# Kernel optimization log

Hardware: AMD Instinct MI355X
Metric: run time of the kernel (lower is better)

Reference implementation:

```python
import jax, jax.numpy as jnp
import numpy as np

B, S, HID = 4, 2048, 2048
H, HKV, D = 16, 4, 128
RANK = 512
SCALE = D ** -0.5


def setup_inputs() -> dict:
    key = jax.random.key(0)
    ks = jax.random.split(key, 5)
    scale_w = 0.02
    return {
        "hidden_states": jax.random.normal(ks[0], (B, S, HID), dtype=jnp.float32),
        "Wq": jax.random.normal(ks[1], (HID, H * D), dtype=jnp.float32) * scale_w,
        "Wc": jax.random.normal(ks[2], (HID, RANK), dtype=jnp.float32) * scale_w,
        "Wup": jax.random.normal(ks[3], (RANK, HKV * D), dtype=jnp.float32) * scale_w,
        "Wo": jax.random.normal(ks[4], (H * D, HID), dtype=jnp.float32) * scale_w,
    }


def reference(hidden_states, Wq, Wc, Wup, Wo):
    b, s, _ = hidden_states.shape
    n_rep = H // HKV
    # Q projection -> (b, H, s, D)
    q = (hidden_states @ Wq).reshape(b, s, H, D).transpose(0, 2, 1, 3)
    # low-rank KV compression -> (b, s, RANK)
    kv_c = hidden_states @ Wc
    # gate in source is ones -> sigmoid(1) constant scalar multiply
    kv_c = kv_c * jax.nn.sigmoid(jnp.float32(1.0))
    # decompress: single kv_up_proj produces shared K/V content
    kv = (kv_c @ Wup).reshape(b, s, HKV, D).transpose(0, 2, 1, 3)  # (b, HKV, s, D)
    k = jnp.repeat(kv, n_rep, axis=1)  # (b, H, s, D), repeat_interleave over heads
    v = k
    scores = jnp.einsum("bhqd,bhkd->bhqk", q, k) * SCALE
    attn = jax.nn.softmax(scores.astype(jnp.float32), axis=-1).astype(q.dtype)
    out = jnp.einsum("bhqk,bhkd->bhqd", attn, v)
    out = out.transpose(0, 2, 1, 3).reshape(b, s, H * D)
    return out @ Wo
```

## Files before the change

### kernel.cpp

```cpp
#include <hip/hip_runtime.h>
#include <hip/hip_bf16.h>
#include <stdint.h>

#define DEV __device__ __forceinline__

typedef __bf16 bf16x8 __attribute__((ext_vector_type(8)));
typedef float f32x4 __attribute__((ext_vector_type(4)));
typedef float f32x16 __attribute__((ext_vector_type(16)));
typedef int i32x4 __attribute__((ext_vector_type(4)));


DEV void gload_lds16(const void* g, void* l) {
  __builtin_amdgcn_global_load_lds((const __attribute__((address_space(1))) void*)g,
                                   (__attribute__((address_space(3))) void*)l, 16, 0, 0);
}

__global__ __launch_bounds__(256) void k_cast(const float* __restrict__ in,
                                              __hip_bfloat16* __restrict__ out, int n) {
  int i = (blockIdx.x * 256 + threadIdx.x) * 8;
  if (i >= n) return;
  const float4* p = (const float4*)(in + i);
  float4 a = p[0], c = p[1];
  bf16x8 v;
  v[0] = (__bf16)a.x; v[1] = (__bf16)a.y; v[2] = (__bf16)a.z; v[3] = (__bf16)a.w;
  v[4] = (__bf16)c.x; v[5] = (__bf16)c.y; v[6] = (__bf16)c.z; v[7] = (__bf16)c.w;
  *(bf16x8*)(out + i) = v;
}

__global__ __launch_bounds__(256) void k_tcast(const float* __restrict__ in,
                                               __hip_bfloat16* __restrict__ out, int R, int C) {
  __shared__ float t[32][33];
  int c0 = blockIdx.x * 32, r0 = blockIdx.y * 32;
  int x = threadIdx.x, y0 = threadIdx.y;
  for (int j = y0; j < 32; j += 8) t[j][x] = in[(size_t)(r0 + j) * C + c0 + x];
  __syncthreads();
  for (int j = y0; j < 32; j += 8)
    out[(size_t)(c0 + j) * R + r0 + x] = __float2bfloat16(t[x][j]);
}

__global__ __launch_bounds__(256) void k_tbf16(const __hip_bfloat16* __restrict__ in,
                                               __hip_bfloat16* __restrict__ out) {
  __shared__ unsigned short t[32][33];
  int z = blockIdx.z;
  const unsigned short* ip = (const unsigned short*)in + (size_t)z * 2048 * 128;
  unsigned short* op = (unsigned short*)out + (size_t)z * 2048 * 128;
  int d0 = blockIdx.x * 32, s0 = blockIdx.y * 32;
  int x = threadIdx.x, y0 = threadIdx.y;
  for (int j = y0; j < 32; j += 8) t[j][x] = ip[(size_t)(s0 + j) * 128 + d0 + x];
  __syncthreads();
  for (int j = y0; j < 32; j += 8) op[(size_t)(d0 + j) * 2048 + s0 + x] = t[x][j];
}

template <int MODE>
__global__ __launch_bounds__(256, 2) void k_gemm(const __hip_bfloat16* __restrict__ A,
                                                 const __hip_bfloat16* __restrict__ BT,
                                                 void* __restrict__ Cout,
                                                 int M, int N, int K, float scale) {
  __shared__ __align__(16) __hip_bfloat16 As[128 * 64];
  __shared__ __align__(16) __hip_bfloat16 Bs[128 * 64];
  const int tid = threadIdx.x;
  const int lane = tid & 63, wid = tid >> 6;
  const int g = lane >> 4, lr = lane & 15;
  const int m0 = blockIdx.x * 128, n0 = blockIdx.y * 128;
  const int wr = wid >> 1, wc = wid & 1;
  const f32x4 vzero = {0.f, 0.f, 0.f, 0.f};

  f32x4 acc[4][4];
#pragma unroll
  for (int i = 0; i < 4; ++i)
#pragma unroll
    for (int j = 0; j < 4; ++j) acc[i][j] = vzero;

  const char* aSrc[4];
  const char* bSrc[4];
  char* aDst[4];
  char* bDst[4];
#pragma unroll
  for (int i = 0; i < 4; ++i) {
    int p = i * 4096 + tid * 16;
    int row = p >> 7, colb = p & 127;
    int scol = colb ^ ((row & 7) << 4);
    aSrc[i] = (const char*)A + ((size_t)(m0 + row) * K) * 2 + scol;
    bSrc[i] = (const char*)BT + ((size_t)(n0 + row) * K) * 2 + scol;
    aDst[i] = (char*)As + i * 4096 + wid * 1024;
    bDst[i] = (char*)Bs + i * 4096 + wid * 1024;
  }

  const int nk = K >> 6;
  for (int kt = 0; kt < nk; ++kt) {
    const size_t ko = (size_t)kt * 128;
#pragma unroll
    for (int i = 0; i < 4; ++i) gload_lds16(aSrc[i] + ko, aDst[i]);
#pragma unroll
    for (int i = 0; i < 4; ++i) gload_lds16(bSrc[i] + ko, bDst[i]);
    __syncthreads();
#pragma unroll
    for (int kc = 0; kc < 2; ++kc) {
      bf16x8 af[4], bfr[4];
#pragma unroll
      for (int fm = 0; fm < 4; ++fm) {
        int row = wr * 64 + fm * 16 + lr;
        int cb = (kc * 64 + g * 16) ^ ((row & 7) << 4);
        af[fm] = *(const bf16x8*)((const char*)As + row * 128 + cb);
      }
#pragma unroll
      for (int fn = 0; fn < 4; ++fn) {
        int row = wc * 64 + fn * 16 + lr;
        int cb = (kc * 64 + g * 16) ^ ((row & 7) << 4);
        bfr[fn] = *(const bf16x8*)((const char*)Bs + row * 128 + cb);
      }
#pragma unroll
      for (int fm = 0; fm < 4; ++fm)
#pragma unroll
        for (int fn = 0; fn < 4; ++fn)
          acc[fm][fn] =
              __builtin_amdgcn_mfma_f32_16x16x32_bf16(af[fm], bfr[fn], acc[fm][fn], 0, 0, 0);
    }
    __syncthreads();
  }

#pragma unroll
  for (int fm = 0; fm < 4; ++fm) {
#pragma unroll
    for (int fn = 0; fn < 4; ++fn) {
      const int mb = m0 + wr * 64 + fm * 16 + g * 4;
      const int n = n0 + wc * 64 + fn * 16 + lr;
#pragma unroll
      for (int r = 0; r < 4; ++r) {
        float v = acc[fm][fn][r] * scale;
        int m = mb + r;
        if constexpr (MODE == 2) {
          int b = m >> 11, s = m & 2047, hk = n >> 7, d = n & 127;
          ((__hip_bfloat16*)Cout)[(((size_t)(b * 4 + hk) * 2048) + s) * 128 + d] =
              __float2bfloat16(v);
        } else {
          ((__hip_bfloat16*)Cout)[(size_t)n * M + m] = __float2bfloat16(v);
        }
      }
    }
  }
}

template <int MODE>
__global__ __launch_bounds__(512, 2) void k_gemm256(const __hip_bfloat16* __restrict__ A,
                                                    const __hip_bfloat16* __restrict__ BT,
                                                    void* __restrict__ Cout,
                                                    int M, int N, int K, float scale) {
  __shared__ __align__(16) char smem[131072];
  const int tid = threadIdx.x;
  const int lane = tid & 63, wid = tid >> 6;
  const int lr = lane & 15, g = lane >> 4;
  const int m0 = blockIdx.x * 256, n0 = blockIdx.y * 256;
  const int wr = wid >> 2, wc = wid & 3;
  const size_t K2 = (size_t)K * 2;
  const f32x4 vzero = {0.f, 0.f, 0.f, 0.f};

  const char *sA0, *sA1, *sB0, *sB1;
  {
    int p = tid * 16;
    int row = p >> 6;
    int slot = (p >> 4) & 3;
    int sw = (slot ^ ((row >> 1) & 3)) << 4;
    sA0 = (const char*)A + (size_t)(m0 + row) * K2 + sw;
    sA1 = (const char*)A + (size_t)(m0 + row + 128) * K2 + sw;
    sB0 = (const char*)BT + (size_t)(n0 + row) * K2 + sw;
    sB1 = (const char*)BT + (size_t)(n0 + row + 128) * K2 + sw;
  }
  char* const ldsW = smem + wid * 1024;

  auto stA = [&](int buf, int kc, size_t koT) {
    char* hb = ldsW + buf * 65536 + kc * 16384;
    gload_lds16(sA0 + koT + (kc << 6), hb);
    gload_lds16(sA1 + koT + (kc << 6), hb + 8192);
  };
  auto stB = [&](int buf, int kc, size_t koT) {
    char* hb = ldsW + buf * 65536 + 32768 + kc * 16384;
    gload_lds16(sB0 + koT + (kc << 6), hb);
    gload_lds16(sB1 + koT + (kc << 6), hb + 8192);
  };

  const int swr = ((g ^ ((lr >> 1) & 3)) << 4);
  const char* rdA = smem + wr * 8192 + lr * 64 + swr;
  const char* rdB = smem + 32768 + wc * 4096 + lr * 64 + swr;

  f32x4 acc[8][4];
#pragma unroll
  for (int i = 0; i < 8; ++i)
#pragma unroll
    for (int j = 0; j < 4; ++j) acc[i][j] = vzero;

  stA(0, 0, 0); stB(0, 0, 0); stA(0, 1, 0); stB(0, 1, 0);

  auto mfma16 = [&](bf16x8* af, bf16x8* bfv, int mh) {
    __builtin_amdgcn_s_setprio(1);
#pragma unroll
    for (int f = 0; f < 4; ++f)
#pragma unroll
      for (int n = 0; n < 4; ++n)
        acc[mh * 4 + f][n] =
            __builtin_amdgcn_mfma_f32_16x16x32_bf16(af[f], bfv[n], acc[mh * 4 + f][n], 0, 0, 0);
    __builtin_amdgcn_s_setprio(0);
  };

  auto tileK = [&](int buf, size_t koNext, bool doStage, bool last) {
    asm volatile("s_waitcnt vmcnt(4)" ::: "memory");
    __builtin_amdgcn_s_barrier();
    bf16x8 a[4], b[4];
    if (doStage) stA(buf ^ 1, 0, koNext);
#pragma unroll
    for (int n = 0; n < 4; ++n) b[n] = *(const bf16x8*)(rdB + buf * 65536 + n * 1024);
#pragma unroll
    for (int f = 0; f < 4; ++f) a[f] = *(const bf16x8*)(rdA + buf * 65536 + f * 1024);
    asm volatile("s_waitcnt lgkmcnt(0)" ::: "memory");
    __builtin_amdgcn_sched_barrier(0);
    mfma16(a, b, 0);
    if (doStage) stB(buf ^ 1, 0, koNext);
#pragma unroll
    for (int f = 0; f < 4; ++f) a[f] = *(const bf16x8*)(rdA + buf * 65536 + 4096 + f * 1024);
    asm volatile("s_waitcnt lgkmcnt(0)" ::: "memory");
    __builtin_amdgcn_sched_barrier(0);
    mfma16(a, b, 1);
    if (last) {
      asm volatile("s_waitcnt vmcnt(0)" ::: "memory");
    } else {
      asm volatile("s_waitcnt vmcnt(4)" ::: "memory");
    }
    __builtin_amdgcn_s_barrier();
    if (doStage) stA(buf ^ 1, 1, koNext);
#pragma unroll
    for (int n = 0; n < 4; ++n) b[n] = *(const bf16x8*)(rdB + buf * 65536 + 16384 + n * 1024);
#pragma unroll
    for (int f = 0; f < 4; ++f) a[f] = *(const bf16x8*)(rdA + buf * 65536 + 16384 + f * 1024);
    asm volatile("s_waitcnt lgkmcnt(0)" ::: "memory");
    __builtin_amdgcn_sched_barrier(0);
    mfma16(a, b, 0);
    if (doStage) stB(buf ^ 1, 1, koNext);
#pragma unroll
    for (int f = 0; f < 4; ++f)
      a[f] = *(const bf16x8*)(rdA + buf * 65536 + 16384 + 4096 + f * 1024);
    asm volatile("s_waitcnt lgkmcnt(0)" ::: "memory");
    __builtin_amdgcn_sched_barrier(0);
    mfma16(a, b, 1);
  };

  const int nk = K >> 6;
  size_t ko = 128;
#pragma unroll 1
  for (int it = 0; it < (nk - 2) / 2; ++it) {
    tileK(0, ko, true, false); ko += 128;
    tileK(1, ko, true, false); ko += 128;
  }
  tileK(0, ko, true, false);
  tileK(1, 0, false, true);

#pragma unroll
  for (int fm = 0; fm < 8; ++fm) {
#pragma unroll
    for (int fn = 0; fn < 4; ++fn) {
      const int mb = m0 + wr * 128 + fm * 16 + g * 4;
      const int n = n0 + wc * 64 + fn * 16 + lr;
#pragma unroll
      for (int r = 0; r < 4; ++r) {
        float v = acc[fm][fn][r] * scale;
        int m = mb + r;
        if constexpr (MODE == 0) {
          ((float*)Cout)[(size_t)m * N + n] = v;
        } else {
          int b = m >> 11, s = m & 2047, h = n >> 7, d = n & 127;
          ((__hip_bfloat16*)Cout)[(((size_t)(b * 16 + h) * 2048) + s) * 128 + d] =
              __float2bfloat16(v);
        }
      }
    }
  }
}

__global__ __launch_bounds__(512, 2) void k_attn2(const __hip_bfloat16* __restrict__ q,
                                                  const __hip_bfloat16* __restrict__ kv,
                                                  const __hip_bfloat16* __restrict__ kvT,
                                                  __hip_bfloat16* __restrict__ out) {
  __shared__ __align__(16) char smem[65536];
  const int tid = threadIdx.x, lane = tid & 63, wid = tid >> 6;
  const int hi = lane >> 5, lq = lane & 31;
  const int qt = blockIdx.x;
  const int pair = blockIdx.y;
  const int b = pair >> 2, hkv = pair & 3;
  const int h = hkv * 4 + (wid & 3);
  const int q0w = qt * 64 + (wid >> 2) * 32;

  const char* qrow =
      (const char*)q + (((size_t)(b * 16 + h) * 2048 + q0w + lq) * 128 + hi * 8) * 2;
  bf16x8 qfr[8];
#pragma unroll
  for (int kt = 0; kt < 8; ++kt) qfr[kt] = *(const bf16x8*)(qrow + kt * 32);

  const char* kbase = (const char*)kv + ((size_t)pair * 2048 * 128) * 2;
  const char* tbase = (const char*)kvT + ((size_t)pair * 2048 * 128) * 2;
  const char* pK;
  const char* pV;
  {
    int p0 = tid * 16;
    int krow = p0 >> 8, kcol = p0 & 255;
    pK = kbase + (size_t)krow * 256 + (kcol ^ ((krow & 15) << 4));
    int vrow = p0 >> 7, vcol = p0 & 127;
    pV = tbase + (size_t)vrow * 4096 + (vcol ^ ((vrow & 7) << 4));
  }

  f32x16 accO[4];
#pragma unroll
  for (int dt = 0; dt < 4; ++dt)
#pragma unroll
    for (int i = 0; i < 16; ++i) accO[dt][i] = 0.f;
  float m_run = -1e30f, l_run = 0.f;

  const int hsK = (hi * 16) ^ ((lq & 15) << 4);
  const int hsV = (hi * 16) ^ ((lq & 7) << 4);

  auto stage = [&](int kb, int vb) {
    gload_lds16(pK, smem + kb + wid * 1024);
    gload_lds16(pK + 8192, smem + kb + 8192 + wid * 1024);
    gload_lds16(pV, smem + vb + wid * 1024);
    gload_lds16(pV + 262144, smem + vb + 8192 + wid * 1024);
    pK += 16384;
    pV += 128;
  };

  auto compute = [&](int kb, int vb) {
    f32x16 st[2];
#pragma unroll
    for (int i = 0; i < 16; ++i) { st[0][i] = 0.f; st[1][i] = 0.f; }
    const char* Kb = smem + kb;
#pragma unroll
    for (int tau = 0; tau < 2; ++tau) {
      const char* Kr = Kb + (tau * 32 + lq) * 256;
#pragma unroll
      for (int kt = 0; kt < 8; ++kt) {
        bf16x8 kf = *(const bf16x8*)(Kr + ((kt * 32) ^ hsK));
        st[tau] = __builtin_amdgcn_mfma_f32_32x32x16_bf16(kf, qfr[kt], st[tau], 0, 0, 0);
      }
    }
    float mloc[8];
#pragma unroll
    for (int i = 0; i < 8; ++i)
      mloc[i] = fmaxf(fmaxf(st[0][i], st[0][i + 8]), fmaxf(st[1][i], st[1][i + 8]));
#pragma unroll
    for (int i = 0; i < 4; ++i) mloc[i] = fmaxf(mloc[i], mloc[i + 4]);
    float pm = fmaxf(fmaxf(mloc[0], mloc[1]), fmaxf(mloc[2], mloc[3]));
    pm = fmaxf(pm, __shfl_xor(pm, 32));
    if (__any(pm > m_run + 8.f)) {
      float mnew = fmaxf(m_run, pm);
      float alpha = __builtin_amdgcn_exp2f(m_run - mnew);
      m_run = mnew;
      l_run *= alpha;
#pragma unroll
      for (int dt = 0; dt < 4; ++dt)
#pragma unroll
        for (int i = 0; i < 16; ++i) accO[dt][i] *= alpha;
    }
    float p0[16], p1[16];
#pragma unroll
    for (int i = 0; i < 16; ++i) p0[i] = __builtin_amdgcn_exp2f(st[0][i] - m_run);
#pragma unroll
    for (int i = 0; i < 16; ++i) p1[i] = __builtin_amdgcn_exp2f(st[1][i] - m_run);
    float s0 = 0.f, s1 = 0.f, s2 = 0.f, s3 = 0.f;
#pragma unroll
    for (int i = 0; i < 8; ++i) {
      s0 += p0[i]; s1 += p0[i + 8]; s2 += p1[i]; s3 += p1[i + 8];
    }
    l_run += (s0 + s1) + (s2 + s3);
    bf16x8 pfr[4];
#pragma unroll
    for (int ks = 0; ks < 4; ++ks) {
      const int base = (ks & 1) * 8;
      int A0, A1, B0, B1;
      if (ks < 2) {
        asm("v_cvt_pk_bf16_f32 %0, %1, %2" : "=v"(A0) : "v"(p0[base + 0]), "v"(p0[base + 1]));
        asm("v_cvt_pk_bf16_f32 %0, %1, %2" : "=v"(A1) : "v"(p0[base + 2]), "v"(p0[base + 3]));
        asm("v_cvt_pk_bf16_f32 %0, %1, %2" : "=v"(B0) : "v"(p0[base + 4]), "v"(p0[base + 5]));
        asm("v_cvt_pk_bf16_f32 %0, %1, %2" : "=v"(B1) : "v"(p0[base + 6]), "v"(p0[base + 7]));
      } else {
        asm("v_cvt_pk_bf16_f32 %0, %1, %2" : "=v"(A0) : "v"(p1[base + 0]), "v"(p1[base + 1]));
        asm("v_cvt_pk_bf16_f32 %0, %1, %2" : "=v"(A1) : "v"(p1[base + 2]), "v"(p1[base + 3]));
        asm("v_cvt_pk_bf16_f32 %0, %1, %2" : "=v"(B0) : "v"(p1[base + 4]), "v"(p1[base + 5]));
        asm("v_cvt_pk_bf16_f32 %0, %1, %2" : "=v"(B1) : "v"(p1[base + 6]), "v"(p1[base + 7]));
      }
      asm("v_permlane32_swap_b32 %0, %1" : "+v"(A0), "+v"(B0));
      asm("v_permlane32_swap_b32 %0, %1" : "+v"(A1), "+v"(B1));
      union { int w[4]; bf16x8 v; } u;
      u.w[0] = A0; u.w[1] = A1; u.w[2] = B0; u.w[3] = B1;
      pfr[ks] = u.v;
    }
    const char* Vb = smem + vb;
#pragma unroll
    for (int dt = 0; dt < 4; ++dt) {
      const char* Vr = Vb + (dt * 32 + lq) * 128;
#pragma unroll
      for (int ks = 0; ks < 4; ++ks) {
        bf16x8 vf = *(const bf16x8*)(Vr + ((ks * 32) ^ hsV));
        accO[dt] = __builtin_amdgcn_mfma_f32_32x32x16_bf16(vf, pfr[ks], accO[dt], 0, 0, 0);
      }
    }
  };

  stage(0, 32768);
  __syncthreads();
#pragma unroll 1
  for (int it = 0; it < 16; ++it) {
    stage(16384, 49152);
    compute(0, 32768);
    __syncthreads();
    if (it < 15) stage(0, 32768);
    compute(16384, 49152);
    __syncthreads();
  }

  float lt = l_run + __shfl_xor(l_run, 32);
  float inv = 1.f / lt;
#pragma unroll
  for (int dt = 0; dt < 4; ++dt)
#pragma unroll
    for (int i = 0; i < 16; ++i) accO[dt][i] *= inv;

  __syncthreads();
  char* scr = smem + wid * 8192;
  const int swq = (lq & 15) << 4;
#pragma unroll
  for (int dt = 0; dt < 4; ++dt) {
#pragma unroll
    for (int rp = 0; rp < 8; ++rp) {
      int w;
      asm("v_cvt_pk_bf16_f32 %0, %1, %2"
          : "=v"(w)
          : "v"(accO[dt][2 * rp]), "v"(accO[dt][2 * rp + 1]));
      int dloc = ((2 * rp) & 3) + 8 * (rp >> 1) + 4 * hi;
      int bytec = (dt * 64 + dloc * 2) ^ swq;
      *(int*)(scr + lq * 256 + bytec) = w;
    }
  }
  __syncthreads();
  const int l16 = lane & 15, lh = lane >> 4;
#pragma unroll
  for (int ps = 0; ps < 8; ++ps) {
    int qr = ps * 4 + lh;
    i32x4 v = *(const i32x4*)(scr + qr * 256 + ((l16 * 16) ^ ((qr & 15) << 4)));
    char* dst = (char*)out + (((size_t)(b * 2048 + q0w + qr) * 2048) + h * 128 + l16 * 8) * 2;
    *(i32x4*)dst = v;
  }
}

extern "C" void kernel_launch(void* const* d_in, const int* in_sizes, int n_in,
                              void* d_out, int out_size, void* d_ws, size_t ws_size,
                              hipStream_t stream) {
  const float* hs = (const float*)d_in[0];
  const float* Wq = (const float*)d_in[1];
  const float* Wc = (const float*)d_in[2];
  const float* Wup = (const float*)d_in[3];
  const float* Wo = (const float*)d_in[4];

  if (ws_size < 105381888u) return;
  char* ws = (char*)d_ws;
  __hip_bfloat16* hs_bf = (__hip_bfloat16*)(ws + 0);
  __hip_bfloat16* q_attn = (__hip_bfloat16*)(ws + 33554432);
  __hip_bfloat16* kvb = (__hip_bfloat16*)(ws + 67108864);
  __hip_bfloat16* kvT = (__hip_bfloat16*)(ws + 75497472);
  __hip_bfloat16* WqT = (__hip_bfloat16*)(ws + 83886080);
  __hip_bfloat16* WoT = (__hip_bfloat16*)(ws + 92274688);
  __hip_bfloat16* WupT = (__hip_bfloat16*)(ws + 100663296);
  __hip_bfloat16* Wc_bf = (__hip_bfloat16*)(ws + 101187584);
  __hip_bfloat16* WckvT = (__hip_bfloat16*)(ws + 103284736);
  __hip_bfloat16* attnout = hs_bf;

  const float qscale = (float)(0.08838834764831845 * 1.4426950408889634);

  k_cast<<<8192, 256, 0, stream>>>(hs, hs_bf, 16777216);
  k_cast<<<512, 256, 0, stream>>>(Wc, Wc_bf, 1048576);
  k_tcast<<<dim3(64, 64), dim3(32, 8), 0, stream>>>(Wq, WqT, 2048, 2048);
  k_tcast<<<dim3(64, 64), dim3(32, 8), 0, stream>>>(Wo, WoT, 2048, 2048);
  k_tcast<<<dim3(16, 16), dim3(32, 8), 0, stream>>>(Wup, WupT, 512, 512);
  k_gemm<3><<<dim3(16, 4), 256, 0, stream>>>(Wc_bf, WupT, WckvT, 2048, 512, 512,
                                             0.7310585786300049f);
  k_gemm256<1><<<dim3(32, 8), 512, 0, stream>>>(hs_bf, WqT, q_attn, 8192, 2048, 2048, qscale);
  k_gemm<2><<<dim3(64, 4), 256, 0, stream>>>(hs_bf, WckvT, kvb, 8192, 512, 2048, 1.0f);
  k_tbf16<<<dim3(4, 64, 16), dim3(32, 8), 0, stream>>>(kvb, kvT);
  k_attn2<<<dim3(32, 16), 512, 0, stream>>>(q_attn, kvb, kvT, attnout);
  k_gemm256<0><<<dim3(32, 8), 512, 0, stream>>>(attnout, WoT, d_out, 8192, 2048, 2048, 1.0f);
}
```

Baseline: 350.8 us.

## Restructure 256x256 GEMM LDS layout, pipeline quadrants, and swizzle block order

New measurement: 353.5 us. Within noise of the previous version (+0.8%).

```diff
diff --git a/kernel.cpp b/kernel.cpp
--- a/kernel.cpp
+++ b/kernel.cpp
@@ -150,38 +150,32 @@
   const int tid = threadIdx.x;
   const int lane = tid & 63, wid = tid >> 6;
   const int lr = lane & 15, g = lane >> 4;
-  const int m0 = blockIdx.x * 256, n0 = blockIdx.y * 256;
+  const int bid = blockIdx.x;
+  const int swz = (bid & 7) * 32 + (bid >> 3);
+  const int m0 = (swz & 31) * 256, n0 = (swz >> 5) * 256;
   const int wr = wid >> 2, wc = wid & 3;
   const size_t K2 = (size_t)K * 2;
   const f32x4 vzero = {0.f, 0.f, 0.f, 0.f};
 
-  const char *sA0, *sA1, *sB0, *sB1;
-  {
-    int p = tid * 16;
-    int row = p >> 6;
-    int slot = (p >> 4) & 3;
-    int sw = (slot ^ ((row >> 1) & 3)) << 4;
-    sA0 = (const char*)A + (size_t)(m0 + row) * K2 + sw;
-    sA1 = (const char*)A + (size_t)(m0 + row + 128) * K2 + sw;
-    sB0 = (const char*)BT + (size_t)(n0 + row) * K2 + sw;
-    sB1 = (const char*)BT + (size_t)(n0 + row + 128) * K2 + sw;
-  }
+  const int srow = tid >> 3, sslot = tid & 7;
+  const int sw = (sslot ^ (srow & 7)) << 4;
+  const char* gA = (const char*)A + (size_t)(m0 + srow) * K2 + sw;
+  const char* gB = (const char*)BT + (size_t)(n0 + srow) * K2 + sw;
+  const size_t hG = (size_t)128 * K2;
+  const size_t r2 = (size_t)64 * K2;
   char* const ldsW = smem + wid * 1024;
 
-  auto stA = [&](int buf, int kc, size_t koT) {
-    char* hb = ldsW + buf * 65536 + kc * 16384;
-    gload_lds16(sA0 + koT + (kc << 6), hb);
-    gload_lds16(sA1 + koT + (kc << 6), hb + 8192);
-  };
-  auto stB = [&](int buf, int kc, size_t koT) {
-    char* hb = ldsW + buf * 65536 + 32768 + kc * 16384;
-    gload_lds16(sB0 + koT + (kc << 6), hb);
-    gload_lds16(sB1 + koT + (kc << 6), hb + 8192);
-  };
-
-  const int swr = ((g ^ ((lr >> 1) & 3)) << 4);
-  const char* rdA = smem + wr * 8192 + lr * 64 + swr;
-  const char* rdB = smem + 32768 + wc * 4096 + lr * 64 + swr;
+  auto stage = [&](int buf, int half, int isB, size_t koB) {
+    const char* src = (isB ? gB : gA) + (half ? hG : 0) + koB;
+    char* dst = ldsW + buf * 65536 + isB * 32768 + half * 16384;
+    gload_lds16(src, dst);
+    gload_lds16(src + r2, dst + 8192);
+  };
+
+  const int sl0 = ((0 + g) ^ (lr & 7)) << 4;
+  const int sl1 = ((4 + g) ^ (lr & 7)) << 4;
+  const char* aB = smem + (wr * 64 + lr) * 128;
+  const char* bB = smem + 32768 + (wc * 32 + lr) * 128;
 
   f32x4 acc[8][4];
 #pragma unroll
@@ -189,80 +183,102 @@
 #pragma unroll
     for (int j = 0; j < 4; ++j) acc[i][j] = vzero;
 
-  stA(0, 0, 0); stB(0, 0, 0); stA(0, 1, 0); stB(0, 1, 0);
-
-  auto mfma16 = [&](bf16x8* af, bf16x8* bfv, int mh) {
+  bf16x8 a[4][2], bl[2][2], bh[2][2];
+  auto ldA = [&](int buf, int half) {
+    const char* p = aB + buf * 65536 + half * 16384;
+#pragma unroll
+    for (int f = 0; f < 4; ++f) {
+      a[f][0] = *(const bf16x8*)(p + f * 2048 + sl0);
+      a[f][1] = *(const bf16x8*)(p + f * 2048 + sl1);
+    }
+  };
+  auto ldB = [&](int buf, int half, bf16x8 (&b)[2][2]) {
+    const char* p = bB + buf * 65536 + half * 16384;
+#pragma unroll
+    for (int n = 0; n < 2; ++n) {
+      b[n][0] = *(const bf16x8*)(p + n * 2048 + sl0);
+      b[n][1] = *(const bf16x8*)(p + n * 2048 + sl1);
+    }
+  };
+  auto mm = [&](bf16x8 (&b)[2][2], int fr, int nc) {
     __builtin_amdgcn_s_setprio(1);
 #pragma unroll
-    for (int f = 0; f < 4; ++f)
-#pragma unroll
-      for (int n = 0; n < 4; ++n)
-        acc[mh * 4 + f][n] =
-            __builtin_amdgcn_mfma_f32_16x16x32_bf16(af[f], bfv[n], acc[mh * 4 + f][n], 0, 0, 0);
+    for (int kc = 0; kc < 2; ++kc)
+#pragma unroll
+      for (int f = 0; f < 4; ++f)
+#pragma unroll
+        for (int n = 0; n < 2; ++n)
+          acc[fr + f][nc + n] = __builtin_amdgcn_mfma_f32_16x16x32_bf16(
+              a[f][kc], b[n][kc], acc[fr + f][nc + n], 0, 0, 0);
     __builtin_amdgcn_s_setprio(0);
   };
 
-  auto tileK = [&](int buf, size_t koNext, bool doStage, bool last) {
-    asm volatile("s_waitcnt vmcnt(4)" ::: "memory");
+  auto tile = [&](int buf, size_t koN, bool st) {
+    ldA(buf, 0);
+    ldB(buf, 0, bl);
+    if (st) {
+      stage(buf ^ 1, 0, 0, koN);
+      asm volatile("s_waitcnt vmcnt(4)" ::: "memory");
+    } else {
+      asm volatile("s_waitcnt vmcnt(2)" ::: "memory");
+    }
     __builtin_amdgcn_s_barrier();
-    bf16x8 a[4], b[4];
-    if (doStage) stA(buf ^ 1, 0, koNext);
-#pragma unroll
-    for (int n = 0; n < 4; ++n) b[n] = *(const bf16x8*)(rdB + buf * 65536 + n * 1024);
-#pragma unroll
-    for (int f = 0; f < 4; ++f) a[f] = *(const bf16x8*)(rdA + buf * 65536 + f * 1024);
     asm volatile("s_waitcnt lgkmcnt(0)" ::: "memory");
     __builtin_amdgcn_sched_barrier(0);
-    mfma16(a, b, 0);
-    if (doStage) stB(buf ^ 1, 0, koNext);
-#pragma unroll
-    for (int f = 0; f < 4; ++f) a[f] = *(const bf16x8*)(rdA + buf * 65536 + 4096 + f * 1024);
+    mm(bl, 0, 0);
+    ldB(buf, 1, bh);
+    if (st) {
+      stage(buf ^ 1, 0, 1, koN);
+      asm volatile("s_waitcnt vmcnt(4)" ::: "memory");
+    } else {
+      asm volatile("s_waitcnt vmcnt(0)" ::: "memory");
+    }
+    __builtin_amdgcn_s_barrier();
     asm volatile("s_waitcnt lgkmcnt(0)" ::: "memory");
     __builtin_amdgcn_sched_barrier(0);
-    mfma16(a, b, 1);
-    if (last) {
-      asm volatile("s_waitcnt vmcnt(0)" ::: "memory");
-    } else {
-      asm volatile("s_waitcnt vmcnt(4)" ::: "memory");
-    }
+    mm(bh, 0, 2);
+    ldA(buf, 1);
+    if (st) stage(buf ^ 1, 1, 1, koN);
     __builtin_amdgcn_s_barrier();
-    if (doStage) stA(buf ^ 1, 1, koNext);
-#pragma unroll
-    for (int n = 0; n < 4; ++n) b[n] = *(const bf16x8*)(rdB + buf * 65536 + 16384 + n * 1024);
-#pragma unroll
-    for (int f = 0; f < 4; ++f) a[f] = *(const bf16x8*)(rdA + buf * 65536 + 16384 + f * 1024);
     asm volatile("s_waitcnt lgkmcnt(0)" ::: "memory");
     __builtin_amdgcn_sched_barrier(0);
-    mfma16(a, b, 0);
-    if (doStage) stB(buf ^ 1, 1, koNext);
-#pragma unroll
-    for (int f = 0; f < 4; ++f)
-      a[f] = *(const bf16x8*)(rdA + buf * 65536 + 16384 + 4096 + f * 1024);
-    asm volatile("s_waitcnt lgkmcnt(0)" ::: "memory");
+    mm(bh, 4, 2);
+    if (st) {
+      stage(buf ^ 1, 1, 0, koN);
+      asm volatile("s_waitcnt vmcnt(4)" ::: "memory");
+    }
+    __builtin_amdgcn_s_barrier();
     __builtin_amdgcn_sched_barrier(0);
-    mfma16(a, b, 1);
-  };
+    mm(bl, 4, 0);
+  };
+
+  stage(0, 0, 0, 0);
+  stage(0, 0, 1, 0);
+  stage(0, 1, 1, 0);
+  stage(0, 1, 0, 0);
+  asm volatile("s_waitcnt vmcnt(4)" ::: "memory");
+  __builtin_amdgcn_s_barrier();
 
   const int nk = K >> 6;
   size_t ko = 128;
 #pragma unroll 1
-  for (int it = 0; it < (nk - 2) / 2; ++it) {
-    tileK(0, ko, true, false); ko += 128;
-    tileK(1, ko, true, false); ko += 128;
-  }
-  tileK(0, ko, true, false);
-  tileK(1, 0, false, true);
+  for (int t = 0; t < nk - 2; t += 2) {
+    tile(0, ko, true); ko += 128;
+    tile(1, ko, true); ko += 128;
+  }
+  tile(0, ko, true);
+  tile(1, 0, false);
 
 #pragma unroll
   for (int fm = 0; fm < 8; ++fm) {
+    const int mrow = m0 + (fm >> 2) * 128 + wr * 64 + (fm & 3) * 16 + g * 4;
 #pragma unroll
     for (int fn = 0; fn < 4; ++fn) {
-      const int mb = m0 + wr * 128 + fm * 16 + g * 4;
-      const int n = n0 + wc * 64 + fn * 16 + lr;
+      const int n = n0 + (fn >> 1) * 128 + wc * 32 + (fn & 1) * 16 + lr;
 #pragma unroll
       for (int r = 0; r < 4; ++r) {
         float v = acc[fm][fn][r] * scale;
-        int m = mb + r;
+        int m = mrow + r;
         if constexpr (MODE == 0) {
           ((float*)Cout)[(size_t)m * N + n] = v;
         } else {
@@ -479,9 +495,9 @@
   k_tcast<<<dim3(16, 16), dim3(32, 8), 0, stream>>>(Wup, WupT, 512, 512);
   k_gemm<3><<<dim3(16, 4), 256, 0, stream>>>(Wc_bf, WupT, WckvT, 2048, 512, 512,
                                              0.7310585786300049f);
-  k_gemm256<1><<<dim3(32, 8), 512, 0, stream>>>(hs_bf, WqT, q_attn, 8192, 2048, 2048, qscale);
+  k_gemm256<1><<<256, 512, 0, stream>>>(hs_bf, WqT, q_attn, 8192, 2048, 2048, qscale);
   k_gemm<2><<<dim3(64, 4), 256, 0, stream>>>(hs_bf, WckvT, kvb, 8192, 512, 2048, 1.0f);
   k_tbf16<<<dim3(4, 64, 16), dim3(32, 8), 0, stream>>>(kvb, kvT);
   k_attn2<<<dim3(32, 16), 512, 0, stream>>>(q_attn, kvb, kvT, attnout);
-  k_gemm256<0><<<dim3(32, 8), 512, 0, stream>>>(attnout, WoT, d_out, 8192, 2048, 2048, 1.0f);
-}
+  k_gemm256<0><<<256, 512, 0, stream>>>(attnout, WoT, d_out, 8192, 2048, 2048, 1.0f);
+}
```
